# Optimization experiments

Measured on AMD Instinct MI355X. Metric: run time of the kernel, lower is better.

Reference implementation:

```python
import jax, jax.numpy as jnp
import numpy as np

EPS = 1e-06


def setup_inputs() -> dict:
    key = jax.random.key(0)
    k1, k2, k3 = jax.random.split(key, 3)
    N, L, H, D = 2, 2048, 8, 64
    return {
        "queries": jax.random.normal(k1, (N, L, H, D), dtype=jnp.float32),
        "keys": jax.random.normal(k2, (N, L, H, D), dtype=jnp.float32),
        "values": jax.random.normal(k3, (N, L, H, D), dtype=jnp.float32),
    }


def reference(queries, keys, values):
    # [N, L, H, D] -> [N, H, L, D]
    q = jnp.transpose(queries, (0, 2, 1, 3))
    k = jnp.transpose(keys, (0, 2, 1, 3))
    v = jnp.transpose(values, (0, 2, 1, 3))
    # kernel_method = sigmoid (applied to q and k only)
    q = jax.nn.sigmoid(q)
    k = jax.nn.sigmoid(k)
    L = q.shape[2]
    normal = (jnp.arange(L, dtype=q.dtype) + 1.0)[None, None, :]  # [1,1,L]

    sink_incoming = 1.0 / jnp.einsum('nhld,nhld->nhl', q + EPS, jnp.cumsum(k, axis=2) + EPS)
    source_outgoing = 1.0 / jnp.einsum('nhld,nhld->nhl', k + EPS, jnp.cumsum(q, axis=2) + EPS)
    sink_incoming = sink_incoming * normal
    source_outgoing = source_outgoing * normal

    conserved_sink = jnp.einsum(
        'nhld,nhld->nhl', q + EPS,
        jnp.cumsum(k * source_outgoing[..., None], axis=2) + EPS) / normal
    conserved_source = jnp.einsum(
        'nhld,nhld->nhl', k + EPS,
        jnp.cumsum(q * sink_incoming[..., None], axis=2) + EPS) / normal
    conserved_source = jnp.clip(conserved_source, -1.0, 1.0)

    sink_allocation = jax.nn.sigmoid(conserved_sink)
    conserved_source = jnp.exp(conserved_source)
    source_competition = conserved_source / jnp.cumsum(conserved_source, axis=-1) * normal

    # causal dot product: outer-product cumsum as in the original
    q_scaled = q * (sink_incoming / normal)[..., None]
    v_scaled = v * source_competition[..., None]
    kv = jnp.cumsum(jnp.einsum('nhld,nhlm->nhldm', k, v_scaled), axis=2)  # [N,H,L,D,M]
    qkv = jnp.einsum('nhld,nhldm->nhlm', q_scaled, kv)
    x = qkv * sink_allocation[..., None]
    # back to [N, L, H, M]
    return jnp.transpose(x, (0, 2, 1, 3))
```

## Files before the change

### kernel.cpp

```cpp
#include <hip/hip_runtime.h>
#include <math.h>

constexpr int Nn = 2, Hh = 8, Ll = 2048, Dd = 64;
constexpr int S  = Nn * Hh;
constexpr int C  = 64;
constexpr int NC = Ll / C;
constexpr int SC = S * NC;

constexpr int SB  = 72;
constexpr int SRP = 65;
constexpr int SS8 = 9;

#define EPSF 1e-6f
#define FLAG_MAGIC 0x5F3A9D21u

typedef __attribute__((ext_vector_type(8))) short short8;
typedef __attribute__((ext_vector_type(4))) float f32x4;
#define MFMA16(a, b, c) __builtin_amdgcn_mfma_f32_16x16x32_bf16(a, b, c, 0, 0, 0)

__device__ __forceinline__ float rcpf(float x) { return __builtin_amdgcn_rcpf(x); }
__device__ __forceinline__ float sigf(float x) { return rcpf(1.0f + __expf(-x)); }

__device__ __forceinline__ float waveRed(float v) {
#pragma unroll
    for (int off = 32; off > 0; off >>= 1) v += __shfl_xor(v, off, 64);
    return v;
}

__device__ __forceinline__ int gidx(int n, int l, int h, int d) {
    return ((n * Ll + l) * Hh + h) * Dd + d;
}

__device__ __forceinline__ float fc(const float4& v, int u) { return ((const float*)&v)[u]; }

__device__ __forceinline__ unsigned short f2bf(float x) {
    unsigned int u = __float_as_uint(x);
    unsigned int r = (u + 0x7fffu + ((u >> 16) & 1u)) >> 16;
    return (unsigned short)r;
}
__device__ __forceinline__ unsigned int pack2(float lo, float hi) {
    return (unsigned int)f2bf(lo) | ((unsigned int)f2bf(hi) << 16);
}
__device__ __forceinline__ float bf2f(unsigned short u) {
    return __uint_as_float(((unsigned int)u) << 16);
}
__device__ __forceinline__ float lo16(unsigned int x) { return __uint_as_float(x << 16); }
__device__ __forceinline__ float hi16(unsigned int x) { return __uint_as_float(x & 0xffff0000u); }
__device__ __forceinline__ void unpack8(const uint4& v, float* o) {
    o[0] = lo16(v.x); o[1] = hi16(v.x); o[2] = lo16(v.y); o[3] = hi16(v.y);
    o[4] = lo16(v.z); o[5] = hi16(v.z); o[6] = lo16(v.w); o[7] = hi16(v.w);
}

__device__ __forceinline__ void pubf(float* p, float v) {
    __hip_atomic_store((unsigned int*)p, __float_as_uint(v),
                       __ATOMIC_RELAXED, __HIP_MEMORY_SCOPE_AGENT);
}
__device__ __forceinline__ float rdf(const float* p) {
    return __uint_as_float(__hip_atomic_load((const unsigned int*)p,
                       __ATOMIC_RELAXED, __HIP_MEMORY_SCOPE_AGENT));
}
__device__ __forceinline__ void pubu(unsigned int* p, unsigned int v) {
    __hip_atomic_store(p, v, __ATOMIC_RELAXED, __HIP_MEMORY_SCOPE_AGENT);
}
__device__ __forceinline__ unsigned long long rd64(const void* p) {
    return __hip_atomic_load((const unsigned long long*)p,
                             __ATOMIC_RELAXED, __HIP_MEMORY_SCOPE_AGENT);
}
__device__ __forceinline__ void publish_flag(unsigned int* f, int t) {
    asm volatile("s_waitcnt vmcnt(0)" ::: "memory");
    __syncthreads();
    if (t == 0)
        __hip_atomic_store(f, FLAG_MAGIC, __ATOMIC_RELAXED, __HIP_MEMORY_SCOPE_AGENT);
}
__device__ __forceinline__ void wait_n(const unsigned int* f, int n, int t) {
    if (t < 64) {
        const bool need = (t < n);
        for (;;) {
            unsigned int v = need
                ? __hip_atomic_load(&f[t], __ATOMIC_RELAXED, __HIP_MEMORY_SCOPE_AGENT)
                : FLAG_MAGIC;
            if (__all(v == FLAG_MAGIC)) break;
            __builtin_amdgcn_s_sleep(8);
        }
    }
    __syncthreads();
    asm volatile("" ::: "memory");
}

__global__ __launch_bounds__(256, 2) void k_all(
        const float* __restrict__ Q, const float* __restrict__ K,
        const float* __restrict__ V,
        float* __restrict__ SK, float* __restrict__ SQ,
        float* __restrict__ SKso, float* __restrict__ SQsi,
        float* __restrict__ KVT, unsigned short* __restrict__ KVpb,
        float* __restrict__ Out,
        unsigned int* __restrict__ f0, unsigned int* __restrict__ f1,
        unsigned long long* __restrict__ f2, unsigned int* __restrict__ f3,
        unsigned int* __restrict__ f4) {
    __shared__ __align__(16) unsigned short sqB[C * SB];
    __shared__ __align__(16) unsigned short skB[C * SB];
    __shared__ __align__(16) unsigned short vsT[C * SB];
    __shared__ __align__(16) unsigned short stB[C * SB];
    __shared__ __align__(16) float Pun[4608];
    __shared__ float scrA[C * SS8], scrB[C * SS8];
    __shared__ float colK[C], colQ[C], pk[Dd], pq[Dd];
    __shared__ float lsi[C], lso[C], rw1[C], rw2[C], le[C], ecum[C], lsc[C], s2l[C];
    __shared__ float pcsv;

    const int b = blockIdx.x, s = b / NC, c = b % NC;
    const int n = s / Hh, h = s % Hh, t = threadIdx.x;
    const int w = t >> 6, lane = t & 63, mf = lane & 15, qq = lane >> 4;
    const int I0 = 16 * w;
    float* P = Pun;

    {
        int d0 = (4 * t) & 63, ig = t >> 4;
        float psk[4] = {0, 0, 0, 0}, psq[4] = {0, 0, 0, 0};
#pragma unroll
        for (int j = 0; j < 4; j++) {
            int i = ig + 16 * j;
            int id = gidx(n, c * C + i, h, d0);
            float4 q4 = *(const float4*)&Q[id];
            float4 k4 = *(const float4*)&K[id];
            float a0 = sigf(q4.x), a1 = sigf(q4.y), a2 = sigf(q4.z), a3 = sigf(q4.w);
            float b0 = sigf(k4.x), b1 = sigf(k4.y), b2 = sigf(k4.z), b3 = sigf(k4.w);
            *(uint2*)&sqB[i * SB + d0] = make_uint2(pack2(a0, a1), pack2(a2, a3));
            *(uint2*)&skB[i * SB + d0] = make_uint2(pack2(b0, b1), pack2(b2, b3));
            psq[0] += a0; psq[1] += a1; psq[2] += a2; psq[3] += a3;
            psk[0] += b0; psk[1] += b1; psk[2] += b2; psk[3] += b3;
        }
#pragma unroll
        for (int r = 0; r < 4; r++) {
            P[ig * 64 + d0 + r] = psk[r];
            P[1024 + ig * 64 + d0 + r] = psq[r];
        }
    }
    __syncthreads();
    if (t < 64) {
        float v = 0.f;
#pragma unroll
        for (int g = 0; g < 16; g++) v += P[g * 64 + t];
        pubf(&SK[b * 64 + t], v);
    } else if (t < 128) {
        int d = t - 64; float v = 0.f;
#pragma unroll
        for (int g = 0; g < 16; g++) v += P[1024 + g * 64 + d];
        pubf(&SQ[b * 64 + d], v);
    }
    publish_flag(&f0[b], t);

    {
        int i0 = (t & 15) * 4, dt = (t >> 4) * 4;
        float4 vr[4];
#pragma unroll
        for (int r = 0; r < 4; r++)
            vr[r] = *(const float4*)&V[gidx(n, c * C + i0 + r, h, dt)];
#pragma unroll
        for (int u = 0; u < 4; u++)
            *(uint2*)&vsT[(dt + u) * SB + i0] = make_uint2(
                pack2(fc(vr[0], u), fc(vr[1], u)), pack2(fc(vr[2], u), fc(vr[3], u)));
    }

#pragma unroll
    for (int j = 0; j < 2; j++) {
        int flat = 8 * t + 2048 * j, i = flat >> 6, d0 = flat & 63;
        uint4 xq = *(const uint4*)&sqB[i * SB + d0];
        uint4 xk = *(const uint4*)&skB[i * SB + d0];
        float qa[8], ka[8];
        unpack8(xq, qa); unpack8(xk, ka);
        float sq = 0.f, sk = 0.f;
#pragma unroll
        for (int u = 0; u < 8; u++) { sq += qa[u]; sk += ka[u]; }
        scrB[i * SS8 + (d0 >> 3)] = sq;
        scrA[i * SS8 + (d0 >> 3)] = sk;
    }
    __syncthreads();
    if (t < 64) {
        float v = 0.f;
#pragma unroll
        for (int u = 0; u < 8; u++) v += scrA[t * SS8 + u];
        colK[t] = v;
    } else if (t < 128) {
        int i = t - 64; float v = 0.f;
#pragma unroll
        for (int u = 0; u < 8; u++) v += scrB[i * SS8 + u];
        colQ[i] = v;
    }
    __syncthreads();

    {
        f32x4 acc[4] = {{0,0,0,0},{0,0,0,0},{0,0,0,0},{0,0,0,0}};
#pragma unroll
        for (int kk = 0; kk < 64; kk += 32) {
            short8 a = *(const short8*)&sqB[(I0 + mf) * SB + kk + qq * 8];
#pragma unroll
            for (int J = 0; J < 4; J++) {
                short8 bb = *(const short8*)&skB[(16 * J + mf) * SB + kk + qq * 8];
                acc[J] = MFMA16(a, bb, acc[J]);
            }
        }
#pragma unroll
        for (int J = 0; J < 4; J++)
#pragma unroll
            for (int r = 0; r < 4; r++)
                P[(I0 + 4 * qq + r) * SRP + 16 * J + mf] = acc[J][r];
    }
    __syncthreads();

    const int bi = t >> 2, bg = t & 3, bl = c * C + bi;
    float prow[16], pcol[16];
    float r1 = 0.f, r2 = 0.f;
#pragma unroll
    for (int u = 0; u < 16; u++) {
        int jj = bg + 4 * u;
        prow[u] = P[bi * SRP + jj] + EPSF * colK[jj];
        pcol[u] = P[jj * SRP + bi] + EPSF * colQ[jj];
        bool ok = (jj <= bi);
        r1 += ok ? prow[u] : 0.f;
        r2 += ok ? pcol[u] : 0.f;
    }
    r1 += __shfl_xor(r1, 1, 64); r1 += __shfl_xor(r1, 2, 64);
    r2 += __shfl_xor(r2, 1, 64); r2 += __shfl_xor(r2, 2, 64);

    wait_n(&f0[s * NC], c, t);

    {
        int d = t & 63, g = t >> 6;
        float pa = 0.f, pb = 0.f;
#pragma unroll
        for (int u = 0; u < 8; u++) {
            int cp = g + 4 * u;
            float va = rdf(&SK[(s * NC + cp) * 64 + d]);
            float vb = rdf(&SQ[(s * NC + cp) * 64 + d]);
            pa += (cp < c) ? va : 0.f;
            pb += (cp < c) ? vb : 0.f;
        }
        scrA[g * 64 + d] = pa;
        scrA[256 + g * 64 + d] = pb;
    }
    __syncthreads();
    if (t < 64) pk[t] = scrA[t] + scrA[64 + t] + scrA[128 + t] + scrA[192 + t];
    else if (t < 128) {
        int d = t - 64;
        pq[d] = scrA[256 + d] + scrA[320 + d] + scrA[384 + d] + scrA[448 + d];
    }
    __syncthreads();
    {
        float b1 = 0.f, b2 = 0.f;
#pragma unroll
        for (int u = 0; u < 16; u++) {
            int d = bg * 16 + u;
            b1 += (bf2f(sqB[bi * SB + d]) + EPSF) * (pk[d] + EPSF);
            b2 += (bf2f(skB[bi * SB + d]) + EPSF) * (pq[d] + EPSF);
        }
        b1 += __shfl_xor(b1, 1, 64); b1 += __shfl_xor(b1, 2, 64);
        b2 += __shfl_xor(b2, 1, 64); b2 += __shfl_xor(b2, 2, 64);
        if (bg == 0) {
            float nf = (float)(bl + 1);
            lsi[bi] = nf * rcpf(b1 + r1);
            lso[bi] = nf * rcpf(b2 + r2);
        }
    }
    __syncthreads();
    {
        int d = t >> 2, g = t & 3;
        float v1 = 0.f, v2 = 0.f;
#pragma unroll
        for (int u = 0; u < 16; u++) {
            int i = g * 16 + u;
            v1 += bf2f(skB[i * SB + d]) * lso[i];
            v2 += bf2f(sqB[i * SB + d]) * lsi[i];
        }
        v1 += __shfl_xor(v1, 1, 64); v1 += __shfl_xor(v1, 2, 64);
        v2 += __shfl_xor(v2, 1, 64); v2 += __shfl_xor(v2, 2, 64);
        if (g == 0) {
            pubf(&SKso[b * 64 + d], v1);
            pubf(&SQsi[b * 64 + d], v2);
        }
    }
    publish_flag(&f1[b], t);

    {
        float a1 = 0.f, a2 = 0.f;
#pragma unroll
        for (int u = 0; u < 16; u++) {
            int jj = bg + 4 * u;
            float t1 = lso[jj] * prow[u];
            float t2 = lsi[jj] * pcol[u];
            bool ok = (jj <= bi);
            a1 += ok ? t1 : 0.f;
            a2 += ok ? t2 : 0.f;
        }
        a1 += __shfl_xor(a1, 1, 64); a1 += __shfl_xor(a1, 2, 64);
        a2 += __shfl_xor(a2, 1, 64); a2 += __shfl_xor(a2, 2, 64);
        if (bg == 0) { rw1[bi] = a1; rw2[bi] = a2; }
    }

    wait_n(&f1[s * NC], c, t);

    {
        int d = t & 63, g = t >> 6;
        float pa = 0.f, pb = 0.f;
#pragma unroll
        for (int u = 0; u < 8; u++) {
            int cp = g + 4 * u;
            float va = rdf(&SKso[(s * NC + cp) * 64 + d]);
            float vb = rdf(&SQsi[(s * NC + cp) * 64 + d]);
            pa += (cp < c) ? va : 0.f;
            pb += (cp < c) ? vb : 0.f;
        }
        scrA[g * 64 + d] = pa;
        scrA[256 + g * 64 + d] = pb;
    }
    __syncthreads();
    if (t < 64) pk[t] = scrA[t] + scrA[64 + t] + scrA[128 + t] + scrA[192 + t];
    else if (t < 128) {
        int d = t - 64;
        pq[d] = scrA[256 + d] + scrA[320 + d] + scrA[384 + d] + scrA[448 + d];
    }
    __syncthreads();
    {
        float b1 = 0.f, b2 = 0.f;
#pragma unroll
        for (int j = 0; j < 2; j++) {
            uint4 xq = *(const uint4*)&sqB[bi * SB + bg * 16 + 8 * j];
            uint4 xk = *(const uint4*)&skB[bi * SB + bg * 16 + 8 * j];
            float qa[8], ka[8];
            unpack8(xq, qa); unpack8(xk, ka);
            int d = bg * 16 + 8 * j;
#pragma unroll
            for (int u = 0; u < 8; u++) {
                b1 += (qa[u] + EPSF) * (pk[d + u] + EPSF);
                b2 += (ka[u] + EPSF) * (pq[d + u] + EPSF);
            }
        }
        b1 += __shfl_xor(b1, 1, 64); b1 += __shfl_xor(b1, 2, 64);
        b2 += __shfl_xor(b2, 1, 64); b2 += __shfl_xor(b2, 2, 64);
        if (bg == 0) {
            float nf = (float)(bl + 1);
            float cs  = (b1 + rw1[bi]) * rcpf(nf);
            float csr = (b2 + rw2[bi]) * rcpf(nf);
            csr = fminf(fmaxf(csr, -1.f), 1.f);
            float e = __expf(csr);
            float sal = sigf(cs);
            s2l[bi] = lsi[bi] * rcpf(nf) * sal;
            le[bi] = e;
        }
    }
    __syncthreads();
    if (t < 64) {
        float run = le[t];
#pragma unroll
        for (int off = 1; off < 64; off <<= 1) {
            float o = __shfl_up(run, off, 64);
            if (t >= off) run += o;
        }
        ecum[t] = run;
    }
    __syncthreads();
    if (t == 0) {
        unsigned long long pv = ((unsigned long long)FLAG_MAGIC << 32)
                              | (unsigned long long)__float_as_uint(ecum[63]);
        __hip_atomic_store(&f2[b], pv, __ATOMIC_RELAXED, __HIP_MEMORY_SCOPE_AGENT);
    }

    if (t < 64) {
        bool need = (t < c);
        float tv = 0.f;
        for (;;) {
            unsigned long long x = need
                ? __hip_atomic_load(&f2[s * NC + t], __ATOMIC_RELAXED, __HIP_MEMORY_SCOPE_AGENT)
                : ((unsigned long long)FLAG_MAGIC << 32);
            if (__all((unsigned int)(x >> 32) == FLAG_MAGIC)) {
                tv = need ? __uint_as_float((unsigned int)x) : 0.f;
                break;
            }
            __builtin_amdgcn_s_sleep(8);
        }
        float v = waveRed(tv);
        if (t == 0) pcsv = v;
    }
    __syncthreads();
    asm volatile("" ::: "memory");

    if (t < 64) {
        int l = c * C + t;
        lsc[t] = le[t] * rcpf(pcsv + ecum[t]) * (float)(l + 1);
    }
    __syncthreads();

    {
        int i = t >> 2, g = t & 3;
        unsigned int wds[8];
#pragma unroll
        for (int p = 0; p < 8; p++) {
            int j0 = g * 16 + 2 * p;
            float v0 = (j0     <= i) ? P[i * SRP + j0]     * lsc[j0]     : 0.f;
            float v1 = (j0 + 1 <= i) ? P[i * SRP + j0 + 1] * lsc[j0 + 1] : 0.f;
            wds[p] = pack2(v0, v1);
        }
        *(uint4*)&stB[i * SB + g * 16]     = make_uint4(wds[0], wds[1], wds[2], wds[3]);
        *(uint4*)&stB[i * SB + g * 16 + 8] = make_uint4(wds[4], wds[5], wds[6], wds[7]);
    }
    __syncthreads();

    unsigned short* skT = (unsigned short*)Pun;
    unsigned short* vsV = (unsigned short*)(Pun + 2304);
#pragma unroll
    for (int j = 0; j < 2; j++) {
        int flat = 8 * t + 2048 * j, dR = flat >> 6, i0 = flat & 63;
        uint4 vv = *(const uint4*)&vsT[dR * SB + i0];
        float x[8];
        unpack8(vv, x);
#pragma unroll
        for (int u = 0; u < 8; u++) x[u] *= lsc[i0 + u];
        uint4 o;
        o.x = pack2(x[0], x[1]); o.y = pack2(x[2], x[3]);
        o.z = pack2(x[4], x[5]); o.w = pack2(x[6], x[7]);
        *(uint4*)&vsV[dR * SB + i0] = o;
    }
    {
        int i0 = (t & 15) * 4, dt = (t >> 4) * 4;
        uint2 kr[4];
#pragma unroll
        for (int r = 0; r < 4; r++) kr[r] = *(const uint2*)&skB[(i0 + r) * SB + dt];
#pragma unroll
        for (int u = 0; u < 4; u++) {
            unsigned int e0 = (u < 2 ? kr[0].x : kr[0].y), e1 = (u < 2 ? kr[1].x : kr[1].y);
            unsigned int e2 = (u < 2 ? kr[2].x : kr[2].y), e3 = (u < 2 ? kr[3].x : kr[3].y);
            int sh = (u & 1) * 16;
            unsigned int lo = ((e0 >> sh) & 0xffffu) | (((e1 >> sh) & 0xffffu) << 16);
            unsigned int hi = ((e2 >> sh) & 0xffffu) | (((e3 >> sh) & 0xffffu) << 16);
            *(uint2*)&skT[(dt + u) * SB + i0] = make_uint2(lo, hi);
        }
    }
    __syncthreads();

    {
        f32x4 acc[4] = {{0,0,0,0},{0,0,0,0},{0,0,0,0},{0,0,0,0}};
#pragma unroll
        for (int kk = 0; kk < 64; kk += 32) {
            short8 a = *(const short8*)&vsV[(I0 + mf) * SB + kk + qq * 8];
#pragma unroll
            for (int J = 0; J < 4; J++) {
                short8 bb = *(const short8*)&skT[(16 * J + mf) * SB + kk + qq * 8];
                acc[J] = MFMA16(a, bb, acc[J]);
            }
        }
#pragma unroll
        for (int J = 0; J < 4; J++)
#pragma unroll
            for (int r = 0; r < 4; r++)
                pubf(&KVT[(size_t)b * 4096 + (I0 + 4 * qq + r) * 64 + 16 * J + mf],
                     acc[J][r]);
    }
    publish_flag(&f3[b], t);

    if (c < 8) {
        wait_n(&f3[s * NC], NC, t);
        int e0 = c * 512 + 2 * t;
        float2 x[NC];
#pragma unroll
        for (int cp = 0; cp < NC; cp++) {
            unsigned long long v = rd64(&KVT[(size_t)(s * NC + cp) * 4096 + e0]);
            x[cp].x = __uint_as_float((unsigned int)v);
            x[cp].y = __uint_as_float((unsigned int)(v >> 32));
        }
        float r0 = 0.f, r1p = 0.f;
#pragma unroll
        for (int cp = 0; cp < NC; cp++) {
            pubu((unsigned int*)&KVpb[(size_t)(s * NC + cp) * 4096 + e0], pack2(r0, r1p));
            r0 += x[cp].x; r1p += x[cp].y;
        }
        publish_flag(&f4[s * 8 + c], t);
    }

    f32x4 acc[4] = {{0,0,0,0},{0,0,0,0},{0,0,0,0},{0,0,0,0}};
#pragma unroll
    for (int kk = 0; kk < 64; kk += 32) {
        short8 a2 = *(const short8*)&stB[(I0 + mf) * SB + kk + qq * 8];
#pragma unroll
        for (int J = 0; J < 4; J++) {
            short8 b2 = *(const short8*)&vsT[(16 * J + mf) * SB + kk + qq * 8];
            acc[J] = MFMA16(a2, b2, acc[J]);
        }
    }

    wait_n(&f4[8 * s], 8, t);
    {
        unsigned long long kvp[4];
        size_t base = (size_t)b * 4096;
#pragma unroll
        for (int j = 0; j < 2; j++) {
            kvp[2 * j]     = rd64(&KVpb[base + 8 * t + 2048 * j]);
            kvp[2 * j + 1] = rd64(&KVpb[base + 8 * t + 2048 * j + 4]);
        }
#pragma unroll
        for (int j = 0; j < 2; j++) {
            int flat = 8 * t + 2048 * j, i = flat >> 6, d0 = flat & 63;
            *(uint2*)&skB[i * SB + d0] =
                make_uint2((unsigned int)kvp[2 * j], (unsigned int)(kvp[2 * j] >> 32));
            *(uint2*)&skB[i * SB + d0 + 4] =
                make_uint2((unsigned int)kvp[2 * j + 1], (unsigned int)(kvp[2 * j + 1] >> 32));
        }
    }
    __syncthreads();

#pragma unroll
    for (int kk = 0; kk < 64; kk += 32) {
        short8 a1 = *(const short8*)&sqB[(I0 + mf) * SB + kk + qq * 8];
#pragma unroll
        for (int J = 0; J < 4; J++) {
            short8 b1 = *(const short8*)&skB[(16 * J + mf) * SB + kk + qq * 8];
            acc[J] = MFMA16(a1, b1, acc[J]);
        }
    }
#pragma unroll
    for (int J = 0; J < 4; J++)
#pragma unroll
        for (int r = 0; r < 4; r++) {
            int io = I0 + 4 * qq + r;
            Out[gidx(n, c * C + io, h, 16 * J + mf)] = acc[J][r] * s2l[io];
        }
}

extern "C" void kernel_launch(void* const* d_in, const int* in_sizes, int n_in,
                              void* d_out, int out_size, void* d_ws, size_t ws_size,
                              hipStream_t stream) {
    const float* Q = (const float*)d_in[0];
    const float* K = (const float*)d_in[1];
    const float* V = (const float*)d_in[2];
    float* Out = (float*)d_out;

    float* ws   = (float*)d_ws;
    float* SK   = ws;
    float* SQ   = SK   + SC * 64;
    float* SKso = SQ   + SC * 64;
    float* SQsi = SKso + SC * 64;
    float* KVT  = SQsi + SC * 64;
    unsigned short* KVpb = (unsigned short*)(KVT + (size_t)SC * 4096);
    unsigned long long* f2 = (unsigned long long*)(KVpb + (size_t)SC * 4096);
    unsigned int* f0 = (unsigned int*)(f2 + SC);
    unsigned int* f1 = f0 + SC;
    unsigned int* f3 = f1 + SC;
    unsigned int* f4 = f3 + SC;

    k_all<<<SC, 256, 0, stream>>>(Q, K, V, SK, SQ, SKso, SQsi, KVT, KVpb, Out,
                                  f0, f1, f2, f3, f4);
}
```

Before: 96.39 us.

## Fold V scaling into MFMA A-operand, transpose K early, publish KV chunk sooner

After: 94.22 us. 1.02x faster.

```diff
diff --git a/kernel.cpp b/kernel.cpp
--- a/kernel.cpp
+++ b/kernel.cpp
@@ -208,6 +208,11 @@
     __syncthreads();
 
     const int bi = t >> 2, bg = t & 3, bl = c * C + bi;
+    const uint4 qrow0 = *(const uint4*)&sqB[bi * SB + bg * 16];
+    const uint4 qrow1 = *(const uint4*)&sqB[bi * SB + bg * 16 + 8];
+    const uint4 krow0 = *(const uint4*)&skB[bi * SB + bg * 16];
+    const uint4 krow1 = *(const uint4*)&skB[bi * SB + bg * 16 + 8];
+
     float prow[16], pcol[16];
     float r1 = 0.f, r2 = 0.f;
 #pragma unroll
@@ -246,12 +251,15 @@
     }
     __syncthreads();
     {
+        float qa[16], ka[16];
+        unpack8(qrow0, qa); unpack8(qrow1, qa + 8);
+        unpack8(krow0, ka); unpack8(krow1, ka + 8);
         float b1 = 0.f, b2 = 0.f;
 #pragma unroll
         for (int u = 0; u < 16; u++) {
             int d = bg * 16 + u;
-            b1 += (bf2f(sqB[bi * SB + d]) + EPSF) * (pk[d] + EPSF);
-            b2 += (bf2f(skB[bi * SB + d]) + EPSF) * (pq[d] + EPSF);
+            b1 += (qa[u] + EPSF) * (pk[d] + EPSF);
+            b2 += (ka[u] + EPSF) * (pq[d] + EPSF);
         }
         b1 += __shfl_xor(b1, 1, 64); b1 += __shfl_xor(b1, 2, 64);
         b2 += __shfl_xor(b2, 1, 64); b2 += __shfl_xor(b2, 2, 64);
@@ -320,19 +328,15 @@
     }
     __syncthreads();
     {
+        float qa[16], ka[16];
+        unpack8(qrow0, qa); unpack8(qrow1, qa + 8);
+        unpack8(krow0, ka); unpack8(krow1, ka + 8);
         float b1 = 0.f, b2 = 0.f;
 #pragma unroll
-        for (int j = 0; j < 2; j++) {
-            uint4 xq = *(const uint4*)&sqB[bi * SB + bg * 16 + 8 * j];
-            uint4 xk = *(const uint4*)&skB[bi * SB + bg * 16 + 8 * j];
-            float qa[8], ka[8];
-            unpack8(xq, qa); unpack8(xk, ka);
-            int d = bg * 16 + 8 * j;
-#pragma unroll
-            for (int u = 0; u < 8; u++) {
-                b1 += (qa[u] + EPSF) * (pk[d + u] + EPSF);
-                b2 += (ka[u] + EPSF) * (pq[d + u] + EPSF);
-            }
+        for (int u = 0; u < 16; u++) {
+            int d = bg * 16 + u;
+            b1 += (qa[u] + EPSF) * (pk[d] + EPSF);
+            b2 += (ka[u] + EPSF) * (pq[d] + EPSF);
         }
         b1 += __shfl_xor(b1, 1, 64); b1 += __shfl_xor(b1, 2, 64);
         b2 += __shfl_xor(b2, 1, 64); b2 += __shfl_xor(b2, 2, 64);
@@ -362,6 +366,22 @@
         unsigned long long pv = ((unsigned long long)FLAG_MAGIC << 32)
                               | (unsigned long long)__float_as_uint(ecum[63]);
         __hip_atomic_store(&f2[b], pv, __ATOMIC_RELAXED, __HIP_MEMORY_SCOPE_AGENT);
+    }
+
+    {
+        int i0 = (t & 15) * 4, dt = (t >> 4) * 4;
+        uint2 kr[4];
+#pragma unroll
+        for (int r = 0; r < 4; r++) kr[r] = *(const uint2*)&skB[(i0 + r) * SB + dt];
+#pragma unroll
+        for (int u = 0; u < 4; u++) {
+            unsigned int e0 = (u < 2 ? kr[0].x : kr[0].y), e1 = (u < 2 ? kr[1].x : kr[1].y);
+            unsigned int e2 = (u < 2 ? kr[2].x : kr[2].y), e3 = (u < 2 ? kr[3].x : kr[3].y);
+            int sh = (u & 1) * 16;
+            unsigned int lo = ((e0 >> sh) & 0xffffu) | (((e1 >> sh) & 0xffffu) << 16);
+            unsigned int hi = ((e2 >> sh) & 0xffffu) | (((e3 >> sh) & 0xffffu) << 16);
+            *(uint2*)&stB[(dt + u) * SB + i0] = make_uint2(lo, hi);
+        }
     }
 
     if (t < 64) {
@@ -390,6 +410,30 @@
     __syncthreads();
 
     {
+        f32x4 acc[4] = {{0,0,0,0},{0,0,0,0},{0,0,0,0},{0,0,0,0}};
+#pragma unroll
+        for (int kk = 0; kk < 64; kk += 32) {
+            short8 av = *(const short8*)&vsT[(I0 + mf) * SB + kk + qq * 8];
+            short8 a;
+#pragma unroll
+            for (int u = 0; u < 8; u++)
+                a[u] = (short)f2bf(bf2f((unsigned short)av[u]) * lsc[kk + qq * 8 + u]);
+#pragma unroll
+            for (int J = 0; J < 4; J++) {
+                short8 bb = *(const short8*)&stB[(16 * J + mf) * SB + kk + qq * 8];
+                acc[J] = MFMA16(a, bb, acc[J]);
+            }
+        }
+#pragma unroll
+        for (int J = 0; J < 4; J++)
+#pragma unroll
+            for (int r = 0; r < 4; r++)
+                pubf(&KVT[(size_t)b * 4096 + (I0 + 4 * qq + r) * 64 + 16 * J + mf],
+                     acc[J][r]);
+    }
+    publish_flag(&f3[b], t);
+
+    {
         int i = t >> 2, g = t & 3;
         unsigned int wds[8];
 #pragma unroll
@@ -403,58 +447,6 @@
         *(uint4*)&stB[i * SB + g * 16 + 8] = make_uint4(wds[4], wds[5], wds[6], wds[7]);
     }
     __syncthreads();
-
-    unsigned short* skT = (unsigned short*)Pun;
-    unsigned short* vsV = (unsigned short*)(Pun + 2304);
-#pragma unroll
-    for (int j = 0; j < 2; j++) {
-        int flat = 8 * t + 2048 * j, dR = flat >> 6, i0 = flat & 63;
-        uint4 vv = *(const uint4*)&vsT[dR * SB + i0];
-        float x[8];
-        unpack8(vv, x);
-#pragma unroll
-        for (int u = 0; u < 8; u++) x[u] *= lsc[i0 + u];
-        uint4 o;
-        o.x = pack2(x[0], x[1]); o.y = pack2(x[2], x[3]);
-        o.z = pack2(x[4], x[5]); o.w = pack2(x[6], x[7]);
-        *(uint4*)&vsV[dR * SB + i0] = o;
-    }
-    {
-        int i0 = (t & 15) * 4, dt = (t >> 4) * 4;
-        uint2 kr[4];
-#pragma unroll
-        for (int r = 0; r < 4; r++) kr[r] = *(const uint2*)&skB[(i0 + r) * SB + dt];
-#pragma unroll
-        for (int u = 0; u < 4; u++) {
-            unsigned int e0 = (u < 2 ? kr[0].x : kr[0].y), e1 = (u < 2 ? kr[1].x : kr[1].y);
-            unsigned int e2 = (u < 2 ? kr[2].x : kr[2].y), e3 = (u < 2 ? kr[3].x : kr[3].y);
-            int sh = (u & 1) * 16;
-            unsigned int lo = ((e0 >> sh) & 0xffffu) | (((e1 >> sh) & 0xffffu) << 16);
-            unsigned int hi = ((e2 >> sh) & 0xffffu) | (((e3 >> sh) & 0xffffu) << 16);
-            *(uint2*)&skT[(dt + u) * SB + i0] = make_uint2(lo, hi);
-        }
-    }
-    __syncthreads();
-
-    {
-        f32x4 acc[4] = {{0,0,0,0},{0,0,0,0},{0,0,0,0},{0,0,0,0}};
-#pragma unroll
-        for (int kk = 0; kk < 64; kk += 32) {
-            short8 a = *(const short8*)&vsV[(I0 + mf) * SB + kk + qq * 8];
-#pragma unroll
-            for (int J = 0; J < 4; J++) {
-                short8 bb = *(const short8*)&skT[(16 * J + mf) * SB + kk + qq * 8];
-                acc[J] = MFMA16(a, bb, acc[J]);
-            }
-        }
-#pragma unroll
-        for (int J = 0; J < 4; J++)
-#pragma unroll
-            for (int r = 0; r < 4; r++)
-                pubf(&KVT[(size_t)b * 4096 + (I0 + 4 * qq + r) * 64 + 16 * J + mf],
-                     acc[J][r]);
-    }
-    publish_flag(&f3[b], t);
 
     if (c < 8) {
         wait_n(&f3[s * NC], NC, t);
```
